# Kernel optimization log

Hardware: AMD Instinct MI355X
Metric: run time of the kernel (lower is better)

The kernel has to match this reference:

```python
import jax, jax.numpy as jnp
import numpy as np

B, N, F_IN = 2, 2048, 256
HEADS, F_OUT = 8, 32
NEG_SLOPE = 0.01  # torch F.leaky_relu default


def setup_inputs() -> dict:
    key = jax.random.key(0)
    k1, k2, k3, k4 = jax.random.split(key, 4)
    stdv = 1.0 / np.sqrt(F_OUT * HEADS)
    h = jax.random.normal(k1, (B, N, F_IN), dtype=jnp.float32)
    adj = jax.random.uniform(k2, (B, N, N), dtype=jnp.float32)
    W = jax.random.normal(k3, (F_IN, F_OUT * HEADS), dtype=jnp.float32) * stdv
    a = jax.random.normal(k4, (2 * F_OUT, 1), dtype=jnp.float32) * stdv
    return {"h": h, "adj": adj, "W": W, "a": a}


def reference(h, adj, W, a):
    # adj is accepted by the original forward but never used (dense attention).
    b, n, _ = h.shape
    f = a.shape[0] // 2
    heads = W.shape[1] // f
    Wh = (h @ W).reshape(b, n, heads, f)            # [b,n,h,f]
    a1 = a[:f, 0]                                    # attends to source i
    a2 = a[f:, 0]                                    # attends to target j
    e1 = jnp.einsum('bnhf,f->bhn', Wh, a1)           # [b,h,n]
    e2 = jnp.einsum('bnhf,f->bhn', Wh, a2)           # [b,h,n]
    # e[b,h,i,j] = leaky_relu(a1.Wh_i + a2.Wh_j) == a^T [Wh_i || Wh_j]
    e = jax.nn.leaky_relu(e1[:, :, :, None] + e2[:, :, None, :], NEG_SLOPE)
    att = jax.nn.softmax(e, axis=-1)                 # softmax over neighbors j
    h_prime = jnp.einsum('bhij,bjhf->bihf', att, Wh)  # [b,n,h,f]
    return h_prime.reshape(b, n, heads * f)
```

## Files before the change

kernel.cpp:

```cpp
#include <hip/hip_runtime.h>
#include <math.h>

#define BATCH 2
#define NTOK  2048
#define FIN   256
#define HEADS 8
#define FOUT  32
#define BH    (BATCH*HEADS)
#define NCOL  (HEADS*FOUT)
#define ROWS  (BATCH*NTOK)

static const size_t OFF_E1   = 1048576;
static const size_t OFF_E2   = OFF_E1 + 32768;
static const size_t OFF_SKEY = OFF_E2 + 32768;
static const size_t OFF_SIDX = OFF_SKEY + 32768;
static const size_t OFF_S1   = OFF_SIDX + 32768;
static const size_t OFF_P2   = OFF_S1 + 32784;
static const size_t OFF_V1   = OFF_P2 + 32784;
static const size_t OFF_P2V  = OFF_V1 + 16u*2049u*32u;
static const size_t OFF_PART = OFF_V1;

__global__ __launch_bounds__(256) void k_gemm(const float* __restrict__ h,
                                              const float* __restrict__ W,
                                              const float* __restrict__ a,
                                              float* __restrict__ Wh,
                                              float* __restrict__ e1,
                                              float* __restrict__ e2) {
    __shared__ float At[64 * 68];
    __shared__ float Bs[64 * 68];
    __shared__ float av[64];
    const int tid  = threadIdx.x;
    const int row0 = blockIdx.x * 64;
    const int col0 = blockIdx.y * 64;
    const int tc = tid & 15;
    const int tr = tid >> 4;
    const int r0 = tr * 4;
    const int c0 = tc * 4;
    if (tid < 64) av[tid] = a[tid];

    const float4* h4 = (const float4*)h;
    const float4* W4 = (const float4*)W;

    float4 acc[4];
    #pragma unroll
    for (int i = 0; i < 4; ++i) acc[i] = make_float4(0.f,0.f,0.f,0.f);

    for (int kc = 0; kc < FIN; kc += 64) {
        #pragma unroll
        for (int q = 0; q < 4; ++q) {
            int idx = q * 256 + tid;
            int r  = idx >> 4;
            int kq = idx & 15;
            float4 v = h4[(size_t)(row0 + r) * 64 + (kc >> 2) + kq];
            At[(kq * 4 + 0) * 68 + r] = v.x;
            At[(kq * 4 + 1) * 68 + r] = v.y;
            At[(kq * 4 + 2) * 68 + r] = v.z;
            At[(kq * 4 + 3) * 68 + r] = v.w;
        }
        #pragma unroll
        for (int q = 0; q < 4; ++q) {
            int idx = q * 256 + tid;
            int kr = idx >> 4;
            int cf = idx & 15;
            float4 v = W4[(size_t)(kc + kr) * 64 + (col0 >> 2) + cf];
            *(float4*)&Bs[kr * 68 + cf * 4] = v;
        }
        __syncthreads();

        #pragma unroll 4
        for (int k = 0; k < 64; ++k) {
            float4 a4 = *(const float4*)&At[k * 68 + r0];
            float4 b4 = *(const float4*)&Bs[k * 68 + c0];
            acc[0].x += a4.x * b4.x; acc[0].y += a4.x * b4.y; acc[0].z += a4.x * b4.z; acc[0].w += a4.x * b4.w;
            acc[1].x += a4.y * b4.x; acc[1].y += a4.y * b4.y; acc[1].z += a4.y * b4.z; acc[1].w += a4.y * b4.w;
            acc[2].x += a4.z * b4.x; acc[2].y += a4.z * b4.y; acc[2].z += a4.z * b4.z; acc[2].w += a4.z * b4.w;
            acc[3].x += a4.w * b4.x; acc[3].y += a4.w * b4.y; acc[3].z += a4.w * b4.z; acc[3].w += a4.w * b4.w;
        }
        __syncthreads();
    }

    #pragma unroll
    for (int i = 0; i < 4; ++i)
        *(float4*)(Wh + (size_t)(row0 + r0 + i) * NCOL + col0 + c0) = acc[i];

    const int f0 = c0 & 31;
    float s1[4], s2[4];
    #pragma unroll
    for (int i = 0; i < 4; ++i) {
        s1[i] = acc[i].x * av[f0+0] + acc[i].y * av[f0+1] + acc[i].z * av[f0+2] + acc[i].w * av[f0+3];
        s2[i] = acc[i].x * av[32+f0+0] + acc[i].y * av[32+f0+1] + acc[i].z * av[32+f0+2] + acc[i].w * av[32+f0+3];
    }
    #pragma unroll
    for (int m = 1; m < 8; m <<= 1) {
        #pragma unroll
        for (int i = 0; i < 4; ++i) {
            s1[i] += __shfl_xor(s1[i], m, 64);
            s2[i] += __shfl_xor(s2[i], m, 64);
        }
    }
    if ((tc & 7) == 0) {
        const int hh = (col0 >> 5) + (tc >> 3);
        #pragma unroll
        for (int i = 0; i < 4; ++i) {
            int grow = row0 + r0 + i;
            int b = grow >> 11;
            int n = grow & (NTOK - 1);
            e1[(b * HEADS + hh) * NTOK + n] = s1[i];
            e2[(b * HEADS + hh) * NTOK + n] = s2[i];
        }
    }
}

__global__ __launch_bounds__(256) void k_rank8(const float* __restrict__ e2g,
                                               int* __restrict__ partial) {
    __shared__ float ch[256];
    const int tid = threadIdx.x;
    const int bh  = blockIdx.x;
    const int jt  = blockIdx.y;
    const int kt  = blockIdx.z;
    ch[tid] = e2g[bh * NTOK + kt * 256 + tid];
    __syncthreads();

    const int j    = jt * 256 + tid;
    const float my = e2g[bh * NTOK + j];
    const int base0 = kt * 256;
    int rank = 0;
    const float4* c4 = (const float4*)ch;
    #pragma unroll 8
    for (int q = 0; q < 64; ++q) {
        float4 v = c4[q];
        int bb = base0 + q * 4;
        rank += (v.x > my) || ((v.x == my) && (bb + 0 < j));
        rank += (v.y > my) || ((v.y == my) && (bb + 1 < j));
        rank += (v.z > my) || ((v.z == my) && (bb + 2 < j));
        rank += (v.w > my) || ((v.w == my) && (bb + 3 < j));
    }
    partial[(kt * BH + bh) * NTOK + j] = rank;
}

__global__ __launch_bounds__(256) void k_scatter(const float* __restrict__ e2g,
                                                 const int* __restrict__ partial,
                                                 float* __restrict__ skey,
                                                 int* __restrict__ sidx) {
    const int tid = threadIdx.x;
    const int bh  = blockIdx.x;
    const int jt  = blockIdx.y;
    const int j   = jt * 256 + tid;
    int rank = 0;
    #pragma unroll
    for (int kt = 0; kt < 8; ++kt)
        rank += partial[(kt * BH + bh) * NTOK + j];
    skey[bh * NTOK + rank] = e2g[bh * NTOK + j];
    sidx[bh * NTOK + rank] = j;
}

__global__ __launch_bounds__(1024) void k_vscan(const float* __restrict__ Wh,
                                                const int* __restrict__ sidx,
                                                const float* __restrict__ skey,
                                                float* __restrict__ V1,
                                                float* __restrict__ P2V,
                                                float* __restrict__ S1,
                                                float* __restrict__ P2) {
    __shared__ float4 wtot[16];
    __shared__ float4 woff[16];
    const int t    = threadIdx.x;
    const int lane = t & 63;
    const int wv   = t >> 6;
    const int fg   = blockIdx.x;
    const int bh   = blockIdx.y;
    const int z    = blockIdx.z;
    const int b    = bh >> 3;
    const int hh   = bh & 7;
    const float scale = z ? 0.01f : 1.0f;

    const int j0 = 2 * t;
    const float w0 = expf(scale * skey[bh * NTOK + j0]);
    const float w1 = expf(scale * skey[bh * NTOK + j0 + 1]);
    float4 v0, v1;
    if (fg < 8) {
        int sj0 = sidx[bh * NTOK + j0];
        int sj1 = sidx[bh * NTOK + j0 + 1];
        float4 g0 = *(const float4*)(Wh + (size_t)(b * NTOK + sj0) * NCOL + hh * FOUT + fg * 4);
        float4 g1 = *(const float4*)(Wh + (size_t)(b * NTOK + sj1) * NCOL + hh * FOUT + fg * 4);
        v0 = make_float4(w0 * g0.x, w0 * g0.y, w0 * g0.z, w0 * g0.w);
        v1 = make_float4(w1 * g1.x, w1 * g1.y, w1 * g1.z, w1 * g1.w);
    } else {
        v0 = make_float4(w0, 0.f, 0.f, 0.f);
        v1 = make_float4(w1, 0.f, 0.f, 0.f);
    }

    float4 s = make_float4(v0.x + v1.x, v0.y + v1.y, v0.z + v1.z, v0.w + v1.w);
    #pragma unroll
    for (int d = 1; d < 64; d <<= 1) {
        float ux = __shfl_up(s.x, (unsigned)d, 64);
        float uy = __shfl_up(s.y, (unsigned)d, 64);
        float uz = __shfl_up(s.z, (unsigned)d, 64);
        float uw = __shfl_up(s.w, (unsigned)d, 64);
        if (lane >= d) { s.x += ux; s.y += uy; s.z += uz; s.w += uw; }
    }
    float4 pair = make_float4(v0.x + v1.x, v0.y + v1.y, v0.z + v1.z, v0.w + v1.w);
    float4 excl = make_float4(s.x - pair.x, s.y - pair.y, s.z - pair.z, s.w - pair.w);
    if (lane == 63) wtot[wv] = s;
    __syncthreads();
    if (t < 16) {
        float4 ws = wtot[t];
        float4 inc = ws;
        #pragma unroll
        for (int d = 1; d < 16; d <<= 1) {
            float ux = __shfl_up(inc.x, (unsigned)d, 16);
            float uy = __shfl_up(inc.y, (unsigned)d, 16);
            float uz = __shfl_up(inc.z, (unsigned)d, 16);
            float uw = __shfl_up(inc.w, (unsigned)d, 16);
            if ((t & 15) >= d) { inc.x += ux; inc.y += uy; inc.z += uz; inc.w += uw; }
        }
        woff[t] = make_float4(inc.x - ws.x, inc.y - ws.y, inc.z - ws.z, inc.w - ws.w);
    }
    __syncthreads();

    float4 base = woff[wv];
    float4 i0 = make_float4(base.x + excl.x + v0.x, base.y + excl.y + v0.y,
                            base.z + excl.z + v0.z, base.w + excl.w + v0.w);
    float4 i1 = make_float4(i0.x + v1.x, i0.y + v1.y, i0.z + v1.z, i0.w + v1.w);

    if (fg < 8) {
        float* dst = z ? P2V : V1;
        *(float4*)(dst + ((size_t)bh * 2049 + (j0 + 1)) * 32 + fg * 4) = i0;
        *(float4*)(dst + ((size_t)bh * 2049 + (j0 + 2)) * 32 + fg * 4) = i1;
        if (t == 0)
            *(float4*)(dst + ((size_t)bh * 2049) * 32 + fg * 4) = make_float4(0.f,0.f,0.f,0.f);
    } else {
        float* dst = z ? P2 : S1;
        dst[bh * 2049 + j0 + 1] = i0.x;
        dst[bh * 2049 + j0 + 2] = i1.x;
        if (t == 0) dst[bh * 2049] = 0.f;
    }
}

__global__ __launch_bounds__(256) void k_out(const float* __restrict__ skey,
                                             const float* __restrict__ e1g,
                                             const float* __restrict__ S1,
                                             const float* __restrict__ P2,
                                             const float* __restrict__ V1,
                                             const float* __restrict__ P2V,
                                             float* __restrict__ out) {
    __shared__ float keys[NTOK];
    const int tid = threadIdx.x;
    const int it  = blockIdx.x;
    const int bh  = blockIdx.y;
    const int b   = bh >> 3;
    const int hh  = bh & 7;
    #pragma unroll
    for (int q = 0; q < 8; ++q)
        keys[q * 256 + tid] = skey[bh * NTOK + q * 256 + tid];
    __syncthreads();

    const int i  = it * 32 + (tid >> 3);
    const int fg = tid & 7;
    const float e1v = e1g[bh * NTOK + i];
    const float th  = -e1v;
    int lo = 0, hi = NTOK;
    while (lo < hi) {
        int mid = (lo + hi) >> 1;
        if (keys[mid] > th) lo = mid + 1; else hi = mid;
    }
    const int k = lo;
    const float A = expf(e1v);
    const float C = expf(0.01f * e1v);
    const float s1  = S1[bh * 2049 + k];
    const float p2k = P2[bh * 2049 + k];
    const float p2t = P2[bh * 2049 + 2048];
    const float l   = A * s1 + C * (p2t - p2k);
    const float inv = 1.0f / l;
    float4 v1   = *(const float4*)(V1  + ((size_t)bh * 2049 + k)    * 32 + fg * 4);
    float4 p2v  = *(const float4*)(P2V + ((size_t)bh * 2049 + k)    * 32 + fg * 4);
    float4 p2vt = *(const float4*)(P2V + ((size_t)bh * 2049 + 2048) * 32 + fg * 4);
    float4 o;
    o.x = (A * v1.x + C * (p2vt.x - p2v.x)) * inv;
    o.y = (A * v1.y + C * (p2vt.y - p2v.y)) * inv;
    o.z = (A * v1.z + C * (p2vt.z - p2v.z)) * inv;
    o.w = (A * v1.w + C * (p2vt.w - p2v.w)) * inv;
    *(float4*)(out + (size_t)(b * NTOK + i) * NCOL + hh * FOUT + fg * 4) = o;
}

extern "C" void kernel_launch(void* const* d_in, const int* in_sizes, int n_in,
                              void* d_out, int out_size, void* d_ws, size_t ws_size,
                              hipStream_t stream) {
    const float* h = (const float*)d_in[0];
    const float* W = (const float*)d_in[2];
    const float* a = (const float*)d_in[3];
    float* out = (float*)d_out;
    float* ws  = (float*)d_ws;

    float* Wh   = ws;
    float* e1   = ws + OFF_E1;
    float* e2   = ws + OFF_E2;
    float* skey = ws + OFF_SKEY;
    int*   sidx = (int*)(ws + OFF_SIDX);
    float* S1   = ws + OFF_S1;
    float* P2   = ws + OFF_P2;
    float* V1   = ws + OFF_V1;
    float* P2V  = ws + OFF_P2V;
    int*   part = (int*)(ws + OFF_PART);

    k_gemm   <<<dim3(ROWS / 64, NCOL / 64), 256, 0, stream>>>(h, W, a, Wh, e1, e2);
    k_rank8  <<<dim3(BH, 8, 8),             256, 0, stream>>>(e2, part);
    k_scatter<<<dim3(BH, 8),                256, 0, stream>>>(e2, part, skey, sidx);
    k_vscan  <<<dim3(9, BH, 2),            1024, 0, stream>>>(Wh, sidx, skey, V1, P2V, S1, P2);
    k_out    <<<dim3(NTOK / 32, BH),        256, 0, stream>>>(skey, e1, S1, P2, V1, P2V, out);
}
```

Baseline: 127.0 us.

## Fuse rank scatter into scan kernel and merge both scan passes

Removes the separate scatter kernel: each scan block sums the partial ranks and scatters keys and indices into shared memory, then one block per head writes the sorted keys out. The two scan passes (scale 1 and 0.01) are merged into one block that gathers each Wh row once and scans both exponential weightings together, halving the gathers and launches. The GEMM A tile is now stored row-major with vector stores instead of a scalar transpose, and the inner loop reads four A rows per k-quad. Every feature-group block now repeats the partial-rank summation and scatter, and the fused scan holds twice as many live registers.

```diff
diff --git a/kernel.cpp b/kernel.cpp
--- a/kernel.cpp
+++ b/kernel.cpp
@@ -13,12 +13,15 @@
 static const size_t OFF_E1   = 1048576;
 static const size_t OFF_E2   = OFF_E1 + 32768;
 static const size_t OFF_SKEY = OFF_E2 + 32768;
-static const size_t OFF_SIDX = OFF_SKEY + 32768;
-static const size_t OFF_S1   = OFF_SIDX + 32768;
+static const size_t OFF_S1   = OFF_SKEY + 32768;
 static const size_t OFF_P2   = OFF_S1 + 32784;
 static const size_t OFF_V1   = OFF_P2 + 32784;
 static const size_t OFF_P2V  = OFF_V1 + 16u*2049u*32u;
-static const size_t OFF_PART = OFF_V1;
+static const size_t OFF_PART = OFF_P2V + 16u*2049u*32u;
+
+#define FMA4(ACC, AV, BV) \
+    ACC.x += (AV) * (BV).x; ACC.y += (AV) * (BV).y; \
+    ACC.z += (AV) * (BV).z; ACC.w += (AV) * (BV).w;
 
 __global__ __launch_bounds__(256) void k_gemm(const float* __restrict__ h,
                                               const float* __restrict__ W,
@@ -26,7 +29,7 @@
                                               float* __restrict__ Wh,
                                               float* __restrict__ e1,
                                               float* __restrict__ e2) {
-    __shared__ float At[64 * 68];
+    __shared__ float As[64 * 68];
     __shared__ float Bs[64 * 68];
     __shared__ float av[64];
     const int tid  = threadIdx.x;
@@ -51,30 +54,33 @@
             int idx = q * 256 + tid;
             int r  = idx >> 4;
             int kq = idx & 15;
-            float4 v = h4[(size_t)(row0 + r) * 64 + (kc >> 2) + kq];
-            At[(kq * 4 + 0) * 68 + r] = v.x;
-            At[(kq * 4 + 1) * 68 + r] = v.y;
-            At[(kq * 4 + 2) * 68 + r] = v.z;
-            At[(kq * 4 + 3) * 68 + r] = v.w;
+            *(float4*)&As[r * 68 + kq * 4] =
+                h4[(size_t)(row0 + r) * 64 + (kc >> 2) + kq];
         }
         #pragma unroll
         for (int q = 0; q < 4; ++q) {
             int idx = q * 256 + tid;
             int kr = idx >> 4;
             int cf = idx & 15;
-            float4 v = W4[(size_t)(kc + kr) * 64 + (col0 >> 2) + cf];
-            *(float4*)&Bs[kr * 68 + cf * 4] = v;
+            *(float4*)&Bs[kr * 68 + cf * 4] =
+                W4[(size_t)(kc + kr) * 64 + (col0 >> 2) + cf];
         }
         __syncthreads();
 
         #pragma unroll 4
-        for (int k = 0; k < 64; ++k) {
-            float4 a4 = *(const float4*)&At[k * 68 + r0];
-            float4 b4 = *(const float4*)&Bs[k * 68 + c0];
-            acc[0].x += a4.x * b4.x; acc[0].y += a4.x * b4.y; acc[0].z += a4.x * b4.z; acc[0].w += a4.x * b4.w;
-            acc[1].x += a4.y * b4.x; acc[1].y += a4.y * b4.y; acc[1].z += a4.y * b4.z; acc[1].w += a4.y * b4.w;
-            acc[2].x += a4.z * b4.x; acc[2].y += a4.z * b4.y; acc[2].z += a4.z * b4.z; acc[2].w += a4.z * b4.w;
-            acc[3].x += a4.w * b4.x; acc[3].y += a4.w * b4.y; acc[3].z += a4.w * b4.z; acc[3].w += a4.w * b4.w;
+        for (int kq = 0; kq < 16; ++kq) {
+            float4 a0 = *(const float4*)&As[(r0 + 0) * 68 + kq * 4];
+            float4 a1 = *(const float4*)&As[(r0 + 1) * 68 + kq * 4];
+            float4 a2 = *(const float4*)&As[(r0 + 2) * 68 + kq * 4];
+            float4 a3 = *(const float4*)&As[(r0 + 3) * 68 + kq * 4];
+            float4 b0 = *(const float4*)&Bs[(kq * 4 + 0) * 68 + c0];
+            float4 b1 = *(const float4*)&Bs[(kq * 4 + 1) * 68 + c0];
+            float4 b2 = *(const float4*)&Bs[(kq * 4 + 2) * 68 + c0];
+            float4 b3 = *(const float4*)&Bs[(kq * 4 + 3) * 68 + c0];
+            FMA4(acc[0], a0.x, b0) FMA4(acc[0], a0.y, b1) FMA4(acc[0], a0.z, b2) FMA4(acc[0], a0.w, b3)
+            FMA4(acc[1], a1.x, b0) FMA4(acc[1], a1.y, b1) FMA4(acc[1], a1.z, b2) FMA4(acc[1], a1.w, b3)
+            FMA4(acc[2], a2.x, b0) FMA4(acc[2], a2.y, b1) FMA4(acc[2], a2.z, b2) FMA4(acc[2], a2.w, b3)
+            FMA4(acc[3], a3.x, b0) FMA4(acc[3], a3.y, b1) FMA4(acc[3], a3.z, b2) FMA4(acc[3], a3.w, b3)
         }
         __syncthreads();
     }
@@ -138,101 +144,133 @@
     partial[(kt * BH + bh) * NTOK + j] = rank;
 }
 
-__global__ __launch_bounds__(256) void k_scatter(const float* __restrict__ e2g,
-                                                 const int* __restrict__ partial,
-                                                 float* __restrict__ skey,
-                                                 int* __restrict__ sidx) {
-    const int tid = threadIdx.x;
-    const int bh  = blockIdx.x;
-    const int jt  = blockIdx.y;
-    const int j   = jt * 256 + tid;
-    int rank = 0;
-    #pragma unroll
-    for (int kt = 0; kt < 8; ++kt)
-        rank += partial[(kt * BH + bh) * NTOK + j];
-    skey[bh * NTOK + rank] = e2g[bh * NTOK + j];
-    sidx[bh * NTOK + rank] = j;
-}
-
-__global__ __launch_bounds__(1024) void k_vscan(const float* __restrict__ Wh,
-                                                const int* __restrict__ sidx,
-                                                const float* __restrict__ skey,
-                                                float* __restrict__ V1,
-                                                float* __restrict__ P2V,
-                                                float* __restrict__ S1,
-                                                float* __restrict__ P2) {
-    __shared__ float4 wtot[16];
-    __shared__ float4 woff[16];
+__global__ __launch_bounds__(1024) void k_scan(const float* __restrict__ e2g,
+                                               const int* __restrict__ partial,
+                                               const float* __restrict__ Wh,
+                                               float* __restrict__ skey,
+                                               float* __restrict__ V1,
+                                               float* __restrict__ P2V,
+                                               float* __restrict__ S1,
+                                               float* __restrict__ P2) {
+    __shared__ float keyS[NTOK];
+    __shared__ int   idxS[NTOK];
+    __shared__ float4 wtot1[16], wtot2[16];
+    __shared__ float4 woff1[16], woff2[16];
     const int t    = threadIdx.x;
     const int lane = t & 63;
     const int wv   = t >> 6;
     const int fg   = blockIdx.x;
     const int bh   = blockIdx.y;
-    const int z    = blockIdx.z;
     const int b    = bh >> 3;
     const int hh   = bh & 7;
-    const float scale = z ? 0.01f : 1.0f;
+
+    #pragma unroll
+    for (int q = 0; q < 2; ++q) {
+        int j = q * 1024 + t;
+        int r = 0;
+        #pragma unroll
+        for (int kt = 0; kt < 8; ++kt)
+            r += partial[(kt * BH + bh) * NTOK + j];
+        keyS[r] = e2g[bh * NTOK + j];
+        idxS[r] = j;
+    }
+    __syncthreads();
+    if (fg == 8) {
+        #pragma unroll
+        for (int q = 0; q < 2; ++q) {
+            int j = q * 1024 + t;
+            skey[bh * NTOK + j] = keyS[j];
+        }
+    }
 
     const int j0 = 2 * t;
-    const float w0 = expf(scale * skey[bh * NTOK + j0]);
-    const float w1 = expf(scale * skey[bh * NTOK + j0 + 1]);
-    float4 v0, v1;
+    float2 kk = *(const float2*)&keyS[j0];
+    int2   sj = *(const int2*)&idxS[j0];
+    float w10 = expf(kk.x), w11 = expf(kk.y);
+    float w20 = expf(0.01f * kk.x), w21 = expf(0.01f * kk.y);
+
+    float4 u0, u1, v0, v1;
     if (fg < 8) {
-        int sj0 = sidx[bh * NTOK + j0];
-        int sj1 = sidx[bh * NTOK + j0 + 1];
-        float4 g0 = *(const float4*)(Wh + (size_t)(b * NTOK + sj0) * NCOL + hh * FOUT + fg * 4);
-        float4 g1 = *(const float4*)(Wh + (size_t)(b * NTOK + sj1) * NCOL + hh * FOUT + fg * 4);
-        v0 = make_float4(w0 * g0.x, w0 * g0.y, w0 * g0.z, w0 * g0.w);
-        v1 = make_float4(w1 * g1.x, w1 * g1.y, w1 * g1.z, w1 * g1.w);
+        float4 g0 = *(const float4*)(Wh + (size_t)(b * NTOK + sj.x) * NCOL + hh * FOUT + fg * 4);
+        float4 g1 = *(const float4*)(Wh + (size_t)(b * NTOK + sj.y) * NCOL + hh * FOUT + fg * 4);
+        u0 = make_float4(w10*g0.x, w10*g0.y, w10*g0.z, w10*g0.w);
+        u1 = make_float4(w11*g1.x, w11*g1.y, w11*g1.z, w11*g1.w);
+        v0 = make_float4(w20*g0.x, w20*g0.y, w20*g0.z, w20*g0.w);
+        v1 = make_float4(w21*g1.x, w21*g1.y, w21*g1.z, w21*g1.w);
     } else {
-        v0 = make_float4(w0, 0.f, 0.f, 0.f);
-        v1 = make_float4(w1, 0.f, 0.f, 0.f);
-    }
-
-    float4 s = make_float4(v0.x + v1.x, v0.y + v1.y, v0.z + v1.z, v0.w + v1.w);
+        u0 = make_float4(w10, 0.f, 0.f, 0.f);
+        u1 = make_float4(w11, 0.f, 0.f, 0.f);
+        v0 = make_float4(w20, 0.f, 0.f, 0.f);
+        v1 = make_float4(w21, 0.f, 0.f, 0.f);
+    }
+
+    float4 s1 = make_float4(u0.x+u1.x, u0.y+u1.y, u0.z+u1.z, u0.w+u1.w);
+    float4 s2 = make_float4(v0.x+v1.x, v0.y+v1.y, v0.z+v1.z, v0.w+v1.w);
+    float4 p1 = s1, p2 = s2;
     #pragma unroll
     for (int d = 1; d < 64; d <<= 1) {
-        float ux = __shfl_up(s.x, (unsigned)d, 64);
-        float uy = __shfl_up(s.y, (unsigned)d, 64);
-        float uz = __shfl_up(s.z, (unsigned)d, 64);
-        float uw = __shfl_up(s.w, (unsigned)d, 64);
-        if (lane >= d) { s.x += ux; s.y += uy; s.z += uz; s.w += uw; }
-    }
-    float4 pair = make_float4(v0.x + v1.x, v0.y + v1.y, v0.z + v1.z, v0.w + v1.w);
-    float4 excl = make_float4(s.x - pair.x, s.y - pair.y, s.z - pair.z, s.w - pair.w);
-    if (lane == 63) wtot[wv] = s;
+        float ax = __shfl_up(s1.x, (unsigned)d, 64);
+        float ay = __shfl_up(s1.y, (unsigned)d, 64);
+        float az = __shfl_up(s1.z, (unsigned)d, 64);
+        float aw = __shfl_up(s1.w, (unsigned)d, 64);
+        float bx = __shfl_up(s2.x, (unsigned)d, 64);
+        float by = __shfl_up(s2.y, (unsigned)d, 64);
+        float bz = __shfl_up(s2.z, (unsigned)d, 64);
+        float bw = __shfl_up(s2.w, (unsigned)d, 64);
+        if (lane >= d) {
+            s1.x += ax; s1.y += ay; s1.z += az; s1.w += aw;
+            s2.x += bx; s2.y += by; s2.z += bz; s2.w += bw;
+        }
+    }
+    float4 ex1 = make_float4(s1.x-p1.x, s1.y-p1.y, s1.z-p1.z, s1.w-p1.w);
+    float4 ex2 = make_float4(s2.x-p2.x, s2.y-p2.y, s2.z-p2.z, s2.w-p2.w);
+    if (lane == 63) { wtot1[wv] = s1; wtot2[wv] = s2; }
     __syncthreads();
     if (t < 16) {
-        float4 ws = wtot[t];
-        float4 inc = ws;
+        float4 a1 = wtot1[t], a2 = wtot2[t];
+        float4 i1 = a1, i2 = a2;
         #pragma unroll
         for (int d = 1; d < 16; d <<= 1) {
-            float ux = __shfl_up(inc.x, (unsigned)d, 16);
-            float uy = __shfl_up(inc.y, (unsigned)d, 16);
-            float uz = __shfl_up(inc.z, (unsigned)d, 16);
-            float uw = __shfl_up(inc.w, (unsigned)d, 16);
-            if ((t & 15) >= d) { inc.x += ux; inc.y += uy; inc.z += uz; inc.w += uw; }
-        }
-        woff[t] = make_float4(inc.x - ws.x, inc.y - ws.y, inc.z - ws.z, inc.w - ws.w);
-    }
-    __syncthreads();
-
-    float4 base = woff[wv];
-    float4 i0 = make_float4(base.x + excl.x + v0.x, base.y + excl.y + v0.y,
-                            base.z + excl.z + v0.z, base.w + excl.w + v0.w);
-    float4 i1 = make_float4(i0.x + v1.x, i0.y + v1.y, i0.z + v1.z, i0.w + v1.w);
+            float ax = __shfl_up(i1.x, (unsigned)d, 16);
+            float ay = __shfl_up(i1.y, (unsigned)d, 16);
+            float az = __shfl_up(i1.z, (unsigned)d, 16);
+            float aw = __shfl_up(i1.w, (unsigned)d, 16);
+            float bx = __shfl_up(i2.x, (unsigned)d, 16);
+            float by = __shfl_up(i2.y, (unsigned)d, 16);
+            float bz = __shfl_up(i2.z, (unsigned)d, 16);
+            float bw = __shfl_up(i2.w, (unsigned)d, 16);
+            if ((t & 15) >= d) {
+                i1.x += ax; i1.y += ay; i1.z += az; i1.w += aw;
+                i2.x += bx; i2.y += by; i2.z += bz; i2.w += bw;
+            }
+        }
+        woff1[t] = make_float4(i1.x-a1.x, i1.y-a1.y, i1.z-a1.z, i1.w-a1.w);
+        woff2[t] = make_float4(i2.x-a2.x, i2.y-a2.y, i2.z-a2.z, i2.w-a2.w);
+    }
+    __syncthreads();
+
+    float4 b1 = woff1[wv], b2 = woff2[wv];
+    float4 i10 = make_float4(b1.x+ex1.x+u0.x, b1.y+ex1.y+u0.y, b1.z+ex1.z+u0.z, b1.w+ex1.w+u0.w);
+    float4 i11 = make_float4(i10.x+u1.x, i10.y+u1.y, i10.z+u1.z, i10.w+u1.w);
+    float4 i20 = make_float4(b2.x+ex2.x+v0.x, b2.y+ex2.y+v0.y, b2.z+ex2.z+v0.z, b2.w+ex2.w+v0.w);
+    float4 i21 = make_float4(i20.x+v1.x, i20.y+v1.y, i20.z+v1.z, i20.w+v1.w);
 
     if (fg < 8) {
-        float* dst = z ? P2V : V1;
-        *(float4*)(dst + ((size_t)bh * 2049 + (j0 + 1)) * 32 + fg * 4) = i0;
-        *(float4*)(dst + ((size_t)bh * 2049 + (j0 + 2)) * 32 + fg * 4) = i1;
-        if (t == 0)
-            *(float4*)(dst + ((size_t)bh * 2049) * 32 + fg * 4) = make_float4(0.f,0.f,0.f,0.f);
+        *(float4*)(V1  + ((size_t)bh * 2049 + (j0 + 1)) * 32 + fg * 4) = i10;
+        *(float4*)(V1  + ((size_t)bh * 2049 + (j0 + 2)) * 32 + fg * 4) = i11;
+        *(float4*)(P2V + ((size_t)bh * 2049 + (j0 + 1)) * 32 + fg * 4) = i20;
+        *(float4*)(P2V + ((size_t)bh * 2049 + (j0 + 2)) * 32 + fg * 4) = i21;
+        if (t == 0) {
+            float4 z4 = make_float4(0.f,0.f,0.f,0.f);
+            *(float4*)(V1  + ((size_t)bh * 2049) * 32 + fg * 4) = z4;
+            *(float4*)(P2V + ((size_t)bh * 2049) * 32 + fg * 4) = z4;
+        }
     } else {
-        float* dst = z ? P2 : S1;
-        dst[bh * 2049 + j0 + 1] = i0.x;
-        dst[bh * 2049 + j0 + 2] = i1.x;
-        if (t == 0) dst[bh * 2049] = 0.f;
+        S1[bh * 2049 + j0 + 1] = i10.x;
+        S1[bh * 2049 + j0 + 2] = i11.x;
+        P2[bh * 2049 + j0 + 1] = i20.x;
+        P2[bh * 2049 + j0 + 2] = i21.x;
+        if (t == 0) { S1[bh * 2049] = 0.f; P2[bh * 2049] = 0.f; }
     }
 }
 
@@ -295,16 +333,14 @@
     float* e1   = ws + OFF_E1;
     float* e2   = ws + OFF_E2;
     float* skey = ws + OFF_SKEY;
-    int*   sidx = (int*)(ws + OFF_SIDX);
     float* S1   = ws + OFF_S1;
     float* P2   = ws + OFF_P2;
     float* V1   = ws + OFF_V1;
     float* P2V  = ws + OFF_P2V;
     int*   part = (int*)(ws + OFF_PART);
 
-    k_gemm   <<<dim3(ROWS / 64, NCOL / 64), 256, 0, stream>>>(h, W, a, Wh, e1, e2);
-    k_rank8  <<<dim3(BH, 8, 8),             256, 0, stream>>>(e2, part);
-    k_scatter<<<dim3(BH, 8),                256, 0, stream>>>(e2, part, skey, sidx);
-    k_vscan  <<<dim3(9, BH, 2),            1024, 0, stream>>>(Wh, sidx, skey, V1, P2V, S1, P2);
-    k_out    <<<dim3(NTOK / 32, BH),        256, 0, stream>>>(skey, e1, S1, P2, V1, P2V, out);
-}
+    k_gemm <<<dim3(ROWS / 64, NCOL / 64), 256, 0, stream>>>(h, W, a, Wh, e1, e2);
+    k_rank8<<<dim3(BH, 8, 8),             256, 0, stream>>>(e2, part);
+    k_scan <<<dim3(9, BH),               1024, 0, stream>>>(e2, part, Wh, skey, V1, P2V, S1, P2);
+    k_out  <<<dim3(NTOK / 32, BH),        256, 0, stream>>>(skey, e1, S1, P2, V1, P2V, out);
+}
```

After: 127.3 us. Within noise of the previous version (+0.2%).
